# Kernel optimization log

Measured on AMD Instinct MI355X. Metric: run time of the kernel, lower is better.

Reference implementation:

```python
import jax, jax.numpy as jnp
import numpy as np

NUM_HEADS = 16
LORA_RANK = 64
LORA_ALPHA = 1.0


def setup_inputs() -> dict:
    key = jax.random.key(0)
    ks = jax.random.split(key, 9)
    B, N, C, r = 16, 1024, 1024, LORA_RANK
    s = lambda k, shp, sc=0.02: (jax.random.normal(k, shp, dtype=jnp.float32) * sc)
    return {
        "x": jax.random.normal(ks[0], (B, N, C), dtype=jnp.float32),
        "W_qkv": s(ks[1], (3 * C, C)),
        "b_qkv": s(ks[2], (3 * C,)),
        "lora_kA": s(ks[3], (r, C), 1.0 / np.sqrt(r)),
        "lora_kB": s(ks[4], (C, r)),
        "lora_vA": s(ks[5], (r, C), 1.0 / np.sqrt(r)),
        "lora_vB": s(ks[6], (C, r)),
        "W_proj": s(ks[7], (C, C)),
        "b_proj": s(ks[8], (C,)),
    }


def reference(x, W_qkv, b_qkv, lora_kA, lora_kB, lora_vA, lora_vB, W_proj, b_proj):
    B, N, C = x.shape
    H = NUM_HEADS
    D = C // H
    scale = D ** -0.5
    lora_scale = LORA_ALPHA / LORA_RANK

    # qkv projection: (B,N,3C)
    qkv = x @ W_qkv.T + b_qkv
    # LoRA deltas for k and v: x @ A.T @ B.T * (alpha/rank)
    k_lora = ((x @ lora_kA.T) @ lora_kB.T) * lora_scale  # (B,N,C)
    v_lora = ((x @ lora_vA.T) @ lora_vB.T) * lora_scale  # (B,N,C)

    qkv = qkv.reshape(B, N, 3, H, D).transpose(2, 0, 3, 1, 4)  # (3,B,H,N,D)
    q, k, v = qkv[0], qkv[1], qkv[2]
    k = k + k_lora.reshape(B, N, H, D).transpose(0, 2, 1, 3)
    v = v + v_lora.reshape(B, N, H, D).transpose(0, 2, 1, 3)

    attn = jnp.einsum('bhqd,bhkd->bhqk', q, k) * scale  # (B,H,N,N)
    attn = jax.nn.softmax(attn, axis=-1)
    out = jnp.einsum('bhqk,bhkd->bhqd', attn, v)  # (B,H,N,D)
    out = out.transpose(0, 2, 1, 3).reshape(B, N, C)
    return out @ W_proj.T + b_proj
```

## Files before the change

kernel.cpp:

```cpp
#include <hip/hip_runtime.h>
#include <hip/hip_bf16.h>
#include <stdint.h>

#define B_  16
#define N_  1024
#define C_  1024
#define H_  16
#define Dh  64
#define M_  (B_*N_)
#define QSCALE (0.125f * 1.44269504f)

typedef __attribute__((ext_vector_type(8)))  short short8;
typedef __attribute__((ext_vector_type(4)))  float f32x4;
typedef __attribute__((ext_vector_type(16))) float f32x16;

__device__ __forceinline__ ushort f2bf(float f) {
  union { float f; uint32_t u; } v; v.f = f;
  uint32_t u = v.u;
  u += 0x7fffu + ((u >> 16) & 1u);
  return (ushort)(u >> 16);
}

__device__ __forceinline__ float exp2fast(float x) {
#if __has_builtin(__builtin_amdgcn_exp2f)
  return __builtin_amdgcn_exp2f(x);
#else
  return exp2f(x);
#endif
}

__device__ __forceinline__ uint32_t pkbf(float lo, float hi) {
  float2 f; f.x = lo; f.y = hi;
  union { __hip_bfloat162 b; uint32_t u; } c;
  c.b = __float22bfloat162_rn(f);
  return c.u;
}

__device__ __forceinline__ void gload_lds16(const ushort* g, ushort* l) {
  __builtin_amdgcn_global_load_lds((const __attribute__((address_space(1))) void*)g,
                                   (__attribute__((address_space(3))) void*)l, 16, 0, 0);
}

struct CastSegs {
  const float* src[7];
  ushort*      dst[7];
  int          cum[7];
  float        scale[7];
};

__global__ void cast_all_k(CastSegs sg, int total4) {
  int i = blockIdx.x * blockDim.x + threadIdx.x;
  int stride = gridDim.x * blockDim.x;
  for (; i < total4; i += stride) {
    int s = 0;
    #pragma unroll
    for (int k = 0; k < 6; ++k) s += (i >= sg.cum[k]);
    int base = s ? sg.cum[s-1] : 0;
    int li = i - base;
    float sc = sg.scale[s];
    float4 v = reinterpret_cast<const float4*>(sg.src[s])[li];
    ushort4 o;
    o.x = f2bf(v.x * sc);
    o.y = f2bf(v.y * sc);
    o.z = f2bf(v.z * sc);
    o.w = f2bf(v.w * sc);
    reinterpret_cast<ushort4*>(sg.dst[s])[li] = o;
  }
}

template<int MODE>
__global__ __launch_bounds__(256)
void gemm128(const ushort* __restrict__ A, int lda,
             const ushort* __restrict__ Bm, int ldb,
             const float* __restrict__ bias,
             const ushort* __restrict__ A2,
             const ushort* __restrict__ B2k, const ushort* __restrict__ B2v,
             ushort* __restrict__ oq, ushort* __restrict__ ok, ushort* __restrict__ ov,
             float* __restrict__ of, int ldo)
{
  __shared__ ushort sA[2][128*32];
  __shared__ ushort sB[2][128*32];
  const int t = threadIdx.x;
  const int lane = t & 63, w = t >> 6;
  const int wr = w >> 1, wc = w & 1;
  const int r = lane & 15, g = lane >> 4;

  int id = blockIdx.x, bx, by;
  if (MODE == 1 || MODE == 2) {
    int pw = id & 63, pm = pw & 15, pn = pw >> 4, P = id >> 6;
    bx = (P & 7) * 16 + pm;
    by = (P >> 3) * 4 + pn;
  } else if (MODE == 3) {
    bx = id & 7; by = id >> 3;
  } else {
    bx = id; by = 0;
  }
  const int m0 = bx * 128, n0 = by * 128;

  const int s = n0 >> 10;
  int nt = 32;
  const ushort* A2b = nullptr; const ushort* B2 = nullptr; int n0loc = 0;
  if (MODE == 1 && s == 1) {
    nt = 34;
    A2b = A2;
    B2 = B2k;
    n0loc = n0 - 1024;
  }
  if (MODE == 3) nt = 34;

  auto stage = [&](int buf, int tt) {
    const ushort* Ab; const ushort* Bb; int ldaT, ldbT;
    if (tt < 32) { Ab = A + m0*lda + tt*32; ldaT = lda; Bb = Bm + n0*ldb + tt*32; ldbT = ldb; }
    else if (MODE == 3) {
      Ab = A2 + m0*64 + (tt-32)*32; ldaT = 64;
      Bb = B2k + n0*128 + (tt-32)*32; ldbT = 128;
    } else {
      Ab = A2b + m0*128 + (tt-32)*32; ldaT = 128;
      Bb = B2 + n0loc*64 + (tt-32)*32; ldbT = 64;
    }
    #pragma unroll
    for (int i = 0; i < 2; ++i) {
      int c = i*256 + t;
      gload_lds16(Ab + (c>>2)*ldaT + (c&3)*8, &sA[buf][c*8]);
      gload_lds16(Bb + (c>>2)*ldbT + (c&3)*8, &sB[buf][c*8]);
    }
  };

  f32x4 acc[4][4];
  #pragma unroll
  for (int i=0;i<4;++i)
    #pragma unroll
    for (int j=0;j<4;++j) acc[i][j] = (f32x4){0.f,0.f,0.f,0.f};

  stage(0, 0);
  for (int tt = 0; tt < nt; ++tt) {
    int cur = tt & 1;
    asm volatile("s_waitcnt vmcnt(0)" ::: "memory");
    __builtin_amdgcn_sched_barrier(0);
    __builtin_amdgcn_s_barrier();
    if (tt + 1 < nt) stage(cur ^ 1, tt + 1);
    short8 af[4], bfr[4];
    #pragma unroll
    for (int i=0;i<4;++i) af[i]  = *(const short8*)&sA[cur][(wr*64 + i*16 + r)*32 + g*8];
    #pragma unroll
    for (int j=0;j<4;++j) bfr[j] = *(const short8*)&sB[cur][(wc*64 + j*16 + r)*32 + g*8];
    #pragma unroll
    for (int i=0;i<4;++i)
      #pragma unroll
      for (int j=0;j<4;++j)
        acc[i][j] = __builtin_amdgcn_mfma_f32_16x16x32_bf16(af[i], bfr[j], acc[i][j], 0,0,0);
  }

  #pragma unroll
  for (int i=0;i<4;++i) {
    #pragma unroll
    for (int j=0;j<4;++j) {
      #pragma unroll
      for (int rr=0;rr<4;++rr) {
        int m = m0 + wr*64 + i*16 + g*4 + rr;
        int n = n0 + wc*64 + j*16 + r;
        float v = acc[i][j][rr];
        if (MODE == 0) {
          oq[m*128 + n] = f2bf(v);
        } else if (MODE == 1) {
          v += bias[n];
          int b = m >> 10, nq = m & 1023;
          int c = n & 1023, h = c >> 6, d = c & 63;
          int idx = ((b*H_ + h)*N_ + nq)*Dh + d;
          if (s == 0)      oq[idx] = f2bf(v * QSCALE);
          else             ok[idx] = f2bf(v);
        } else if (MODE == 3) {
          v += bias[m];
          int h = m >> 6, d = m & 63;
          int b = n >> 10, nq = n & 1023;
          ov[((b*H_ + h)*Dh + d)*N_ + nq] = f2bf(v);
        } else {
          of[m*ldo + n] = v + bias[n];
        }
      }
    }
  }
}

__global__ __launch_bounds__(256, 4)
void flash_attn32(const ushort* __restrict__ qb, const ushort* __restrict__ kb,
                  const ushort* __restrict__ vb, ushort* __restrict__ out)
{
  __shared__ ushort Kt[2][64*64];
  __shared__ ushort Vt[2][64*64];
  const int t = threadIdx.x, w = t >> 6, lane = t & 63;
  const int ql = lane & 31, hi = lane >> 5;

  int bid = (blockIdx.x & 7) * 256 + (blockIdx.x >> 3);
  const int bh = bid >> 3, qt = bid & 7;
  const int b = bh >> 4, h = bh & 15;
  const ushort* Q  = qb + bh * (N_*Dh);
  const ushort* K  = kb + bh * (N_*Dh);
  const ushort* VT = vb + bh * (Dh*N_);
  const int q0 = qt*128 + w*32;

  short8 qf[4];
  #pragma unroll
  for (int ds=0; ds<4; ++ds)
    qf[ds] = *(const short8*)&Q[(q0 + ql)*Dh + ds*16 + hi*8];

  f32x16 o0, o1;
  #pragma unroll
  for (int r=0;r<16;++r) { o0[r]=0.f; o1[r]=0.f; }
  float lsum = 0.f;

  const int srow = t >> 3, scc = (t & 7) ^ ((t >> 3) & 7);
  const ushort* Ksrc0 = K  + srow*Dh + scc*8;
  const ushort* Vsrc0 = VT + srow*N_ + scc*8;
  ushort* Kdst = &Kt[0][t*8];
  ushort* Vdst = &Vt[0][t*8];

  const int km = ql & 7;
  int off[4];
  #pragma unroll
  for (int i=0;i<4;++i) off[i] = ql*64 + (((i*2 + hi) ^ km) * 8);

  auto stage = [&](int buf, int kt) {
    const ushort* Kp = Ksrc0 + kt*(64*Dh);
    const ushort* Vp = Vsrc0 + kt*64;
    gload_lds16(Kp,          Kdst + buf*4096);
    gload_lds16(Kp + 32*Dh,  Kdst + buf*4096 + 2048);
    gload_lds16(Vp,          Vdst + buf*4096);
    gload_lds16(Vp + 32*N_,  Vdst + buf*4096 + 2048);
  };

  auto tile = [&](const int cur, const int kt) {
    asm volatile("s_waitcnt vmcnt(0)" ::: "memory");
    __builtin_amdgcn_sched_barrier(0);
    __builtin_amdgcn_s_barrier();
    if (kt < 15) stage(cur ^ 1, kt + 1);

    f32x16 s0, s1;
    #pragma unroll
    for (int r=0;r<16;++r) { s0[r]=0.f; s1[r]=0.f; }
    __builtin_amdgcn_s_setprio(1);
    #pragma unroll
    for (int ds=0; ds<4; ++ds) {
      short8 kfA = *(const short8*)&Kt[cur][off[ds]];
      short8 kfB = *(const short8*)&Kt[cur][off[ds] + 2048];
      s0 = __builtin_amdgcn_mfma_f32_32x32x16_bf16(kfA, qf[ds], s0, 0,0,0);
      s1 = __builtin_amdgcn_mfma_f32_32x32x16_bf16(kfB, qf[ds], s1, 0,0,0);
    }
    __builtin_amdgcn_s_setprio(0);

    #pragma unroll
    for (int sg=0; sg<4; ++sg) {
      const int rb = (sg & 1) * 8;
      float e0,e1,e2,e3,e4,e5,e6,e7;
      if (sg < 2) {
        e0=exp2fast(s0[rb+0]); e1=exp2fast(s0[rb+1]);
        e2=exp2fast(s0[rb+2]); e3=exp2fast(s0[rb+3]);
        e4=exp2fast(s0[rb+4]); e5=exp2fast(s0[rb+5]);
        e6=exp2fast(s0[rb+6]); e7=exp2fast(s0[rb+7]);
      } else {
        e0=exp2fast(s1[rb+0]); e1=exp2fast(s1[rb+1]);
        e2=exp2fast(s1[rb+2]); e3=exp2fast(s1[rb+3]);
        e4=exp2fast(s1[rb+4]); e5=exp2fast(s1[rb+5]);
        e6=exp2fast(s1[rb+6]); e7=exp2fast(s1[rb+7]);
      }
      lsum += ((e0+e1)+(e2+e3)) + ((e4+e5)+(e6+e7));
      uint32_t w01 = pkbf(e0, e1);
      uint32_t w23 = pkbf(e2, e3);
      uint32_t w45 = pkbf(e4, e5);
      uint32_t w67 = pkbf(e6, e7);
      uint32_t t0 = hi ? w01 : w45;
      uint32_t t1 = hi ? w23 : w67;
      uint32_t xt0 = __shfl_xor(t0, 32);
      uint32_t xt1 = __shfl_xor(t1, 32);
      union { uint32_t u[4]; short8 s8; } pu;
      pu.u[0] = hi ? xt0 : w01;
      pu.u[1] = hi ? xt1 : w23;
      pu.u[2] = hi ? w45 : xt0;
      pu.u[3] = hi ? w67 : xt1;
      short8 pf = pu.s8;

      short8 vfA = *(const short8*)&Vt[cur][off[sg]];
      short8 vfB = *(const short8*)&Vt[cur][off[sg] + 2048];
      __builtin_amdgcn_s_setprio(1);
      o0 = __builtin_amdgcn_mfma_f32_32x32x16_bf16(pf, vfA, o0, 0,0,0);
      o1 = __builtin_amdgcn_mfma_f32_32x32x16_bf16(pf, vfB, o1, 0,0,0);
      __builtin_amdgcn_s_setprio(0);
    }
  };

  stage(0, 0);
  for (int ktp = 0; ktp < 16; ktp += 2) {
    tile(0, ktp);
    tile(1, ktp + 1);
  }

  float lfull = lsum + __shfl_xor(lsum, 32);
  float inv = 1.f / lfull;
  #pragma unroll
  for (int r=0;r<16;++r) {
    int qr = (r&3) + 8*(r>>2) + 4*hi;
    float invr = __shfl(inv, qr);
    int row = b*N_ + q0 + qr;
    out[row*C_ + h*Dh + ql]      = f2bf(o0[r] * invr);
    out[row*C_ + h*Dh + 32 + ql] = f2bf(o1[r] * invr);
  }
}

extern "C" void kernel_launch(void* const* d_in, const int* in_sizes, int n_in,
                              void* d_out, int out_size, void* d_ws, size_t ws_size,
                              hipStream_t stream)
{
  const float* x      = (const float*)d_in[0];
  const float* W_qkv  = (const float*)d_in[1];
  const float* b_qkv  = (const float*)d_in[2];
  const float* kA     = (const float*)d_in[3];
  const float* kB     = (const float*)d_in[4];
  const float* vA     = (const float*)d_in[5];
  const float* vB     = (const float*)d_in[6];
  const float* W_proj = (const float*)d_in[7];
  const float* b_proj = (const float*)d_in[8];
  float* out = (float*)d_out;

  ushort* ws    = (ushort*)d_ws;
  ushort* xb    = ws;
  ushort* wqkvb = xb + 16777216;
  ushort* kvAb  = wqkvb + 3145728;
  ushort* kBb   = kvAb + 131072;
  ushort* vBb   = kBb + 65536;
  ushort* wprojb= vBb + 65536;
  ushort* tkv   = wprojb + 1048576;
  ushort* qbuf  = tkv + 2097152;
  ushort* kbuf  = qbuf + 16777216;
  ushort* vbuf  = kbuf + 16777216;
  ushort* attn  = xb;

  const float ls = 1.0f / 64.0f;

  CastSegs sg;
  const float* srcs[7] = { x, W_qkv, kA, vA, kB, vB, W_proj };
  ushort* dsts[7]      = { xb, wqkvb, kvAb, kvAb + 65536, kBb, vBb, wprojb };
  int     n4s[7]       = { 16777216/4, 3145728/4, 65536/4, 65536/4, 65536/4, 65536/4, 1048576/4 };
  float   scs[7]       = { 1.f, 1.f, 1.f, 1.f, ls, ls, 1.f };
  int cum = 0;
  for (int i = 0; i < 7; ++i) {
    sg.src[i] = srcs[i]; sg.dst[i] = dsts[i]; sg.scale[i] = scs[i];
    cum += n4s[i]; sg.cum[i] = cum;
  }
  cast_all_k<<<dim3(4096), dim3(256), 0, stream>>>(sg, cum);

  gemm128<0><<<dim3(128), dim3(256), 0, stream>>>(
      xb, 1024, kvAb, 1024, nullptr, nullptr, nullptr, nullptr,
      tkv, nullptr, nullptr, nullptr, 0);

  gemm128<1><<<dim3(2048), dim3(256), 0, stream>>>(
      xb, 1024, wqkvb, 1024, b_qkv, tkv, kBb, nullptr,
      qbuf, kbuf, nullptr, nullptr, 0);

  gemm128<3><<<dim3(1024), dim3(256), 0, stream>>>(
      wqkvb + 2048*1024, 1024, xb, 1024, b_qkv + 2048, vBb, tkv + 64, nullptr,
      nullptr, nullptr, vbuf, nullptr, 0);

  flash_attn32<<<dim3(2048), dim3(256), 0, stream>>>(qbuf, kbuf, vbuf, attn);

  gemm128<2><<<dim3(1024), dim3(256), 0, stream>>>(
      attn, 1024, wprojb, 1024, b_proj, nullptr, nullptr, nullptr,
      nullptr, nullptr, nullptr, out, 1024);
}
```

Baseline: 342.2 us.

## Fuse x fp32-to-bf16 cast into the LoRA-A projection GEMM

The x cast moves out of the generic cast kernel and into a new LoRA-A GEMM. That GEMM loads fp32 x, converts it to bf16 in registers, writes it to both LDS and the global bf16 buffer, and computes x·[kA;vA]^T. This removes one full pass of reading the fp32 activation and then rereading the bf16 copy, and it drops a kernel launch. The risk is that the fused kernel runs on only 128 blocks, so the 64MB fp32 read is spread over few CUs and may be bandwidth-limited per block.

```diff
diff --git a/kernel.cpp b/kernel.cpp
--- a/kernel.cpp
+++ b/kernel.cpp
@@ -42,10 +42,10 @@
 }
 
 struct CastSegs {
-  const float* src[7];
-  ushort*      dst[7];
-  int          cum[7];
-  float        scale[7];
+  const float* src[6];
+  ushort*      dst[6];
+  int          cum[6];
+  float        scale[6];
 };
 
 __global__ void cast_all_k(CastSegs sg, int total4) {
@@ -54,7 +54,7 @@
   for (; i < total4; i += stride) {
     int s = 0;
     #pragma unroll
-    for (int k = 0; k < 6; ++k) s += (i >= sg.cum[k]);
+    for (int k = 0; k < 5; ++k) s += (i >= sg.cum[k]);
     int base = s ? sg.cum[s-1] : 0;
     int li = i - base;
     float sc = sg.scale[s];
@@ -66,6 +66,101 @@
     o.w = f2bf(v.w * sc);
     reinterpret_cast<ushort4*>(sg.dst[s])[li] = o;
   }
+}
+
+__global__ __launch_bounds__(256)
+void lora1_cast_k(const float* __restrict__ xf, const ushort* __restrict__ kvAb,
+                  ushort* __restrict__ xb, ushort* __restrict__ tkv)
+{
+  __shared__ ushort sA[2][128*32];
+  __shared__ ushort sB[2][128*32];
+  const int t = threadIdx.x;
+  const int lane = t & 63, w = t >> 6;
+  const int wr = w >> 1, wc = w & 1;
+  const int r = lane & 15, g = lane >> 4;
+  const int m0 = blockIdx.x * 128;
+
+  const int rowA0 = t >> 2, kcA = (t & 3) * 8;
+  const int rowA1 = rowA0 + 64;
+  const float* xA0 = xf + (m0 + rowA0) * 1024 + kcA;
+  const float* xA1 = xf + (m0 + rowA1) * 1024 + kcA;
+  ushort* xbA0 = xb + (m0 + rowA0) * 1024 + kcA;
+  ushort* xbA1 = xb + (m0 + rowA1) * 1024 + kcA;
+
+  float4 fa[4];
+  auto loadA = [&](int tt) {
+    fa[0] = *(const float4*)(xA0 + tt*32);
+    fa[1] = *(const float4*)(xA0 + tt*32 + 4);
+    fa[2] = *(const float4*)(xA1 + tt*32);
+    fa[3] = *(const float4*)(xA1 + tt*32 + 4);
+  };
+  auto stageB = [&](int buf, int tt) {
+    #pragma unroll
+    for (int i = 0; i < 2; ++i) {
+      int c = i*256 + t;
+      gload_lds16(kvAb + (c>>2)*1024 + tt*32 + (c&3)*8, &sB[buf][c*8]);
+    }
+  };
+  auto writeA = [&](int buf, int tt) {
+    union { ushort u[8]; short8 s8; } p0, p1;
+    p0.u[0]=f2bf(fa[0].x); p0.u[1]=f2bf(fa[0].y); p0.u[2]=f2bf(fa[0].z); p0.u[3]=f2bf(fa[0].w);
+    p0.u[4]=f2bf(fa[1].x); p0.u[5]=f2bf(fa[1].y); p0.u[6]=f2bf(fa[1].z); p0.u[7]=f2bf(fa[1].w);
+    p1.u[0]=f2bf(fa[2].x); p1.u[1]=f2bf(fa[2].y); p1.u[2]=f2bf(fa[2].z); p1.u[3]=f2bf(fa[2].w);
+    p1.u[4]=f2bf(fa[3].x); p1.u[5]=f2bf(fa[3].y); p1.u[6]=f2bf(fa[3].z); p1.u[7]=f2bf(fa[3].w);
+    *(short8*)&sA[buf][t*8]        = p0.s8;
+    *(short8*)&sA[buf][(t+256)*8]  = p1.s8;
+    *(short8*)(xbA0 + tt*32) = p0.s8;
+    *(short8*)(xbA1 + tt*32) = p1.s8;
+  };
+
+  f32x4 acc[4][4];
+  #pragma unroll
+  for (int i=0;i<4;++i)
+    #pragma unroll
+    for (int j=0;j<4;++j) acc[i][j] = (f32x4){0.f,0.f,0.f,0.f};
+
+  loadA(0);
+  stageB(0, 0);
+  asm volatile("s_waitcnt vmcnt(0)" ::: "memory");
+  writeA(0, 0);
+  asm volatile("s_waitcnt lgkmcnt(0)" ::: "memory");
+  __builtin_amdgcn_sched_barrier(0);
+  __builtin_amdgcn_s_barrier();
+
+  for (int tt = 0; tt < 32; ++tt) {
+    int cur = tt & 1;
+    if (tt < 31) { loadA(tt + 1); stageB(cur ^ 1, tt + 1); }
+
+    short8 af[4], bfr[4];
+    #pragma unroll
+    for (int i=0;i<4;++i) af[i]  = *(const short8*)&sA[cur][(wr*64 + i*16 + r)*32 + g*8];
+    #pragma unroll
+    for (int j=0;j<4;++j) bfr[j] = *(const short8*)&sB[cur][(wc*64 + j*16 + r)*32 + g*8];
+    #pragma unroll
+    for (int i=0;i<4;++i)
+      #pragma unroll
+      for (int j=0;j<4;++j)
+        acc[i][j] = __builtin_amdgcn_mfma_f32_16x16x32_bf16(af[i], bfr[j], acc[i][j], 0,0,0);
+
+    if (tt < 31) {
+      asm volatile("s_waitcnt vmcnt(0)" ::: "memory");
+      writeA(cur ^ 1, tt + 1);
+    }
+    asm volatile("s_waitcnt lgkmcnt(0)" ::: "memory");
+    __builtin_amdgcn_sched_barrier(0);
+    __builtin_amdgcn_s_barrier();
+  }
+
+  #pragma unroll
+  for (int i=0;i<4;++i)
+    #pragma unroll
+    for (int j=0;j<4;++j)
+      #pragma unroll
+      for (int rr=0;rr<4;++rr) {
+        int m = m0 + wr*64 + i*16 + g*4 + rr;
+        int n = wc*64 + j*16 + r;
+        tkv[m*128 + n] = f2bf(acc[i][j][rr]);
+      }
 }
 
 template<int MODE>
@@ -90,10 +185,8 @@
     int pw = id & 63, pm = pw & 15, pn = pw >> 4, P = id >> 6;
     bx = (P & 7) * 16 + pm;
     by = (P >> 3) * 4 + pn;
-  } else if (MODE == 3) {
+  } else {
     bx = id & 7; by = id >> 3;
-  } else {
-    bx = id; by = 0;
   }
   const int m0 = bx * 128, n0 = by * 128;
 
@@ -160,9 +253,7 @@
         int m = m0 + wr*64 + i*16 + g*4 + rr;
         int n = n0 + wc*64 + j*16 + r;
         float v = acc[i][j][rr];
-        if (MODE == 0) {
-          oq[m*128 + n] = f2bf(v);
-        } else if (MODE == 1) {
+        if (MODE == 1) {
           v += bias[n];
           int b = m >> 10, nq = m & 1023;
           int c = n & 1023, h = c >> 6, d = c & 63;
@@ -337,20 +428,18 @@
   const float ls = 1.0f / 64.0f;
 
   CastSegs sg;
-  const float* srcs[7] = { x, W_qkv, kA, vA, kB, vB, W_proj };
-  ushort* dsts[7]      = { xb, wqkvb, kvAb, kvAb + 65536, kBb, vBb, wprojb };
-  int     n4s[7]       = { 16777216/4, 3145728/4, 65536/4, 65536/4, 65536/4, 65536/4, 1048576/4 };
-  float   scs[7]       = { 1.f, 1.f, 1.f, 1.f, ls, ls, 1.f };
+  const float* srcs[6] = { W_qkv, kA, vA, kB, vB, W_proj };
+  ushort* dsts[6]      = { wqkvb, kvAb, kvAb + 65536, kBb, vBb, wprojb };
+  int     n4s[6]       = { 3145728/4, 65536/4, 65536/4, 65536/4, 65536/4, 1048576/4 };
+  float   scs[6]       = { 1.f, 1.f, 1.f, ls, ls, 1.f };
   int cum = 0;
-  for (int i = 0; i < 7; ++i) {
+  for (int i = 0; i < 6; ++i) {
     sg.src[i] = srcs[i]; sg.dst[i] = dsts[i]; sg.scale[i] = scs[i];
     cum += n4s[i]; sg.cum[i] = cum;
   }
-  cast_all_k<<<dim3(4096), dim3(256), 0, stream>>>(sg, cum);
-
-  gemm128<0><<<dim3(128), dim3(256), 0, stream>>>(
-      xb, 1024, kvAb, 1024, nullptr, nullptr, nullptr, nullptr,
-      tkv, nullptr, nullptr, nullptr, 0);
+  cast_all_k<<<dim3(2048), dim3(256), 0, stream>>>(sg, cum);
+
+  lora1_cast_k<<<dim3(128), dim3(256), 0, stream>>>(x, kvAb, xb, tkv);
 
   gemm128<1><<<dim3(2048), dim3(256), 0, stream>>>(
       xb, 1024, wqkvb, 1024, b_qkv, tkv, kBb, nullptr,
```

New measurement: 356.2 us. 1.04x slower.

## Fold LoRA deltas into W_qkv weights instead of computing per-token LoRA path

Applied to the files above, without the earlier changes.

Instead of computing x@A^T per token and adding the rank-64 LoRA contribution via extra K-tiles in the QKV GEMMs, the code precomputes B@A (scaled) and adds it in place to the bf16 K and V rows of W_qkv with a small GEMM. The cast kernel writes transposed copies of the A matrices for this. This removes the 16K-row x@A GEMM and two extra K-iterations per QKV tile. In exchange the merged weight is rounded to bf16 twice, once when cast and once after the add, which slightly changes precision.

```diff
diff --git a/kernel.cpp b/kernel.cpp
--- a/kernel.cpp
+++ b/kernel.cpp
@@ -19,6 +19,10 @@
   uint32_t u = v.u;
   u += 0x7fffu + ((u >> 16) & 1u);
   return (ushort)(u >> 16);
+}
+
+__device__ __forceinline__ float bf2f(ushort us) {
+  union { uint32_t u; float f; } c; c.u = ((uint32_t)us) << 16; return c.f;
 }
 
 __device__ __forceinline__ float exp2fast(float x) {
@@ -64,7 +68,17 @@
     o.y = f2bf(v.y * sc);
     o.z = f2bf(v.z * sc);
     o.w = f2bf(v.w * sc);
-    reinterpret_cast<ushort4*>(sg.dst[s])[li] = o;
+    if (s < 5) {
+      reinterpret_cast<ushort4*>(sg.dst[s])[li] = o;
+    } else {
+      int e0 = li * 4;
+      int r = e0 >> 10, j = e0 & 1023;
+      ushort* d = sg.dst[s];
+      d[(j+0)*64 + r] = o.x;
+      d[(j+1)*64 + r] = o.y;
+      d[(j+2)*64 + r] = o.z;
+      d[(j+3)*64 + r] = o.w;
+    }
   }
 }
 
@@ -74,7 +88,7 @@
              const ushort* __restrict__ Bm, int ldb,
              const float* __restrict__ bias,
              const ushort* __restrict__ A2,
-             const ushort* __restrict__ B2k, const ushort* __restrict__ B2v,
+             const ushort* __restrict__ B2,
              ushort* __restrict__ oq, ushort* __restrict__ ok, ushort* __restrict__ ov,
              float* __restrict__ of, int ldo)
 {
@@ -85,7 +99,7 @@
   const int wr = w >> 1, wc = w & 1;
   const int r = lane & 15, g = lane >> 4;
 
-  int id = blockIdx.x, bx, by;
+  int id = blockIdx.x, bx, by, half = 0;
   if (MODE == 1 || MODE == 2) {
     int pw = id & 63, pm = pw & 15, pn = pw >> 4, P = id >> 6;
     bx = (P & 7) * 16 + pm;
@@ -93,36 +107,25 @@
   } else if (MODE == 3) {
     bx = id & 7; by = id >> 3;
   } else {
-    bx = id; by = 0;
+    half = id >> 6;
+    int lid = id & 63;
+    bx = lid >> 3; by = lid & 7;
   }
   const int m0 = bx * 128, n0 = by * 128;
-
   const int s = n0 >> 10;
-  int nt = 32;
-  const ushort* A2b = nullptr; const ushort* B2 = nullptr; int n0loc = 0;
-  if (MODE == 1 && s == 1) {
-    nt = 34;
-    A2b = A2;
-    B2 = B2k;
-    n0loc = n0 - 1024;
-  }
-  if (MODE == 3) nt = 34;
+  const int nt = (MODE == 4) ? 2 : 32;
+
+  const ushort* Ause = A;  const ushort* Buse = Bm;
+  if (MODE == 4 && half) { Ause = A2; Buse = B2; }
 
   auto stage = [&](int buf, int tt) {
-    const ushort* Ab; const ushort* Bb; int ldaT, ldbT;
-    if (tt < 32) { Ab = A + m0*lda + tt*32; ldaT = lda; Bb = Bm + n0*ldb + tt*32; ldbT = ldb; }
-    else if (MODE == 3) {
-      Ab = A2 + m0*64 + (tt-32)*32; ldaT = 64;
-      Bb = B2k + n0*128 + (tt-32)*32; ldbT = 128;
-    } else {
-      Ab = A2b + m0*128 + (tt-32)*32; ldaT = 128;
-      Bb = B2 + n0loc*64 + (tt-32)*32; ldbT = 64;
-    }
+    const ushort* Ab = Ause + m0*lda + tt*32;
+    const ushort* Bb = Buse + n0*ldb + tt*32;
     #pragma unroll
     for (int i = 0; i < 2; ++i) {
       int c = i*256 + t;
-      gload_lds16(Ab + (c>>2)*ldaT + (c&3)*8, &sA[buf][c*8]);
-      gload_lds16(Bb + (c>>2)*ldbT + (c&3)*8, &sB[buf][c*8]);
+      gload_lds16(Ab + (c>>2)*lda + (c&3)*8, &sA[buf][c*8]);
+      gload_lds16(Bb + (c>>2)*ldb + (c&3)*8, &sB[buf][c*8]);
     }
   };
 
@@ -160,9 +163,7 @@
         int m = m0 + wr*64 + i*16 + g*4 + rr;
         int n = n0 + wc*64 + j*16 + r;
         float v = acc[i][j][rr];
-        if (MODE == 0) {
-          oq[m*128 + n] = f2bf(v);
-        } else if (MODE == 1) {
+        if (MODE == 1) {
           v += bias[n];
           int b = m >> 10, nq = m & 1023;
           int c = n & 1023, h = c >> 6, d = c & 63;
@@ -174,6 +175,9 @@
           int h = m >> 6, d = m & 63;
           int b = n >> 10, nq = n & 1023;
           ov[((b*H_ + h)*Dh + d)*N_ + nq] = f2bf(v);
+        } else if (MODE == 4) {
+          ushort* p = oq + (1024 + half*1024 + m)*1024 + n;
+          *p = f2bf(bf2f(*p) + v);
         } else {
           of[m*ldo + n] = v + bias[n];
         }
@@ -324,12 +328,12 @@
   ushort* ws    = (ushort*)d_ws;
   ushort* xb    = ws;
   ushort* wqkvb = xb + 16777216;
-  ushort* kvAb  = wqkvb + 3145728;
-  ushort* kBb   = kvAb + 131072;
+  ushort* kAt   = wqkvb + 3145728;
+  ushort* vAt   = kAt + 65536;
+  ushort* kBb   = vAt + 65536;
   ushort* vBb   = kBb + 65536;
   ushort* wprojb= vBb + 65536;
-  ushort* tkv   = wprojb + 1048576;
-  ushort* qbuf  = tkv + 2097152;
+  ushort* qbuf  = wprojb + 1048576;
   ushort* kbuf  = qbuf + 16777216;
   ushort* vbuf  = kbuf + 16777216;
   ushort* attn  = xb;
@@ -337,10 +341,11 @@
   const float ls = 1.0f / 64.0f;
 
   CastSegs sg;
-  const float* srcs[7] = { x, W_qkv, kA, vA, kB, vB, W_proj };
-  ushort* dsts[7]      = { xb, wqkvb, kvAb, kvAb + 65536, kBb, vBb, wprojb };
-  int     n4s[7]       = { 16777216/4, 3145728/4, 65536/4, 65536/4, 65536/4, 65536/4, 1048576/4 };
-  float   scs[7]       = { 1.f, 1.f, 1.f, 1.f, ls, ls, 1.f };
+  const float* srcs[7] = { x, W_qkv, kBb ? kB : kB, vB, W_proj, kA, vA };
+  ushort* dsts[7]      = { xb, wqkvb, kBb, vBb, wprojb, kAt, vAt };
+  int     n4s[7]       = { 16777216/4, 3145728/4, 65536/4, 65536/4, 1048576/4, 65536/4, 65536/4 };
+  float   scs[7]       = { 1.f, 1.f, ls, ls, 1.f, 1.f, 1.f };
+  srcs[2] = kB;
   int cum = 0;
   for (int i = 0; i < 7; ++i) {
     sg.src[i] = srcs[i]; sg.dst[i] = dsts[i]; sg.scale[i] = scs[i];
@@ -348,21 +353,21 @@
   }
   cast_all_k<<<dim3(4096), dim3(256), 0, stream>>>(sg, cum);
 
-  gemm128<0><<<dim3(128), dim3(256), 0, stream>>>(
-      xb, 1024, kvAb, 1024, nullptr, nullptr, nullptr, nullptr,
-      tkv, nullptr, nullptr, nullptr, 0);
+  gemm128<4><<<dim3(128), dim3(256), 0, stream>>>(
+      kBb, 64, kAt, 64, nullptr, vBb, vAt,
+      wqkvb, nullptr, nullptr, nullptr, 0);
 
   gemm128<1><<<dim3(2048), dim3(256), 0, stream>>>(
-      xb, 1024, wqkvb, 1024, b_qkv, tkv, kBb, nullptr,
+      xb, 1024, wqkvb, 1024, b_qkv, nullptr, nullptr,
       qbuf, kbuf, nullptr, nullptr, 0);
 
   gemm128<3><<<dim3(1024), dim3(256), 0, stream>>>(
-      wqkvb + 2048*1024, 1024, xb, 1024, b_qkv + 2048, vBb, tkv + 64, nullptr,
+      wqkvb + 2048*1024, 1024, xb, 1024, b_qkv + 2048, nullptr, nullptr,
       nullptr, nullptr, vbuf, nullptr, 0);
 
   flash_attn32<<<dim3(2048), dim3(256), 0, stream>>>(qbuf, kbuf, vbuf, attn);
 
   gemm128<2><<<dim3(1024), dim3(256), 0, stream>>>(
-      attn, 1024, wprojb, 1024, b_proj, nullptr, nullptr, nullptr,
+      attn, 1024, wprojb, 1024, b_proj, nullptr, nullptr,
       nullptr, nullptr, nullptr, out, 1024);
 }
```

Result: slower. 362.1 us (+5.8%).
